# Performance work log

Measured on AMD Instinct MI355X. Metric: run time of the kernel, lower is better.

The kernel has to match this reference:

```python
import jax, jax.numpy as jnp
import numpy as np

N, E = 50000, 800000          # nodes, edges
D_IN, D_HID, D_OUT = 128, 128, 64


def setup_inputs() -> dict:
    key = jax.random.key(0)
    ks = jax.random.split(key, 8)
    init = lambda k, s: (jax.random.normal(k, s, jnp.float32) / np.sqrt(s[0]).astype(np.float32))
    return dict(
        x=jax.random.normal(ks[0], (N, D_IN), jnp.float32),
        edge_index=jax.random.randint(ks[1], (2, E), 0, N, dtype=jnp.int64),
        edge_attr=jax.random.uniform(ks[2], (E,), jnp.float32),
        W1=init(ks[3], (D_IN, D_HID)), b1=jnp.zeros((D_HID,), jnp.float32),
        W2=init(ks[4], (D_HID, D_HID)), b2=jnp.zeros((D_HID,), jnp.float32),
        Wmu=init(ks[5], (D_HID, D_OUT)), bmu=jnp.zeros((D_OUT,), jnp.float32),
        Wstd=init(ks[6], (D_HID, D_OUT)), bstd=jnp.zeros((D_OUT,), jnp.float32),
    )


def gcn_conv(x, src, dst, ew, W, b):
    """PyG GCNConv: symmetric-normalized aggregation with self-loops (weight 1).
    Self-loop contribution handled analytically (dinv[i]^2 * h[i]) to avoid
    concatenating N extra edges."""
    h = x @ W                                              # [N, Dout]
    deg = jax.ops.segment_sum(ew, dst, num_segments=N) + 1.0   # +1 for self-loop
    dinv = jnp.where(deg > 0, deg ** -0.5, 0.0)            # D^{-1/2}
    norm = dinv[src] * ew * dinv[dst]                      # [E]
    agg = jax.ops.segment_sum(h[src] * norm[:, None], dst, num_segments=N)
    agg = agg + h * (dinv * dinv)[:, None]                 # self-loop term
    return agg + b


def reference(x, edge_index, edge_attr, W1, b1, W2, b2, Wmu, bmu, Wstd, bstd):
    src, dst = edge_index[0], edge_index[1]
    h = jax.nn.relu(gcn_conv(x, src, dst, edge_attr, W1, b1))   # encoder layer 1
    h = gcn_conv(h, src, dst, edge_attr, W2, b2)                # encoder layer 2
    h = jax.nn.relu(h)                                          # .relu() in forward
    mu = gcn_conv(h, src, dst, edge_attr, Wmu, bmu)
    std = gcn_conv(h, src, dst, edge_attr, Wstd, bstd)
    return mu, std
```

## Files before the change

kernel.cpp:

```cpp
#include <hip/hip_runtime.h>
#include <math.h>

static constexpr int N = 50000;
static constexpr int E = 800000;
static constexpr int D = 128;
static constexpr int DO = 64;
static constexpr int CAP = 64;

__device__ __forceinline__ unsigned pack_bf16(float a, float b) {
  unsigned ua = __float_as_uint(a), ub = __float_as_uint(b);
  ua = (ua + 0x7FFFu + ((ua >> 16) & 1u)) >> 16;
  ub = (ub + 0x7FFFu + ((ub >> 16) & 1u)) >> 16;
  return ua | (ub << 16);
}
__device__ __forceinline__ float blo(unsigned u) { return __uint_as_float(u << 16); }
__device__ __forceinline__ float bhi(unsigned u) { return __uint_as_float(u & 0xFFFF0000u); }

typedef __attribute__((ext_vector_type(8))) short bf16x8;
typedef __attribute__((ext_vector_type(4))) float f32x4;

__global__ __launch_bounds__(256) void k_zero(int* __restrict__ cnt) {
  int i = blockIdx.x * 256 + threadIdx.x;
  if (i < N) cnt[i] = 0;
}

__global__ __launch_bounds__(256) void k_build_ell(const int* __restrict__ src,
                                                   const int* __restrict__ dst,
                                                   const float* __restrict__ ew,
                                                   int* __restrict__ cnt,
                                                   int2* __restrict__ ell) {
  int e = blockIdx.x * 256 + threadIdx.x;
  if (e >= E) return;
  int s = src[e], d = dst[e];
  int pos = __hip_atomic_fetch_add(&cnt[d], 1, __ATOMIC_RELAXED, __HIP_MEMORY_SCOPE_AGENT);
  if (pos < CAP)
    ell[(size_t)d * CAP + pos] = make_int2(s, __float_as_int(ew[e]));
}

__global__ __launch_bounds__(256) void k_degcast(const float* __restrict__ x,
                                                 const int* __restrict__ cnt,
                                                 const int2* __restrict__ ell,
                                                 float* __restrict__ dinv,
                                                 unsigned* __restrict__ bhs) {
  int node = blockIdx.x * 4 + (threadIdx.x >> 6);
  if (node >= N) return;
  int lane = threadIdx.x & 63;

  int len = cnt[node];
  float sum = (lane < len) ? __int_as_float(ell[(size_t)node * CAP + lane].y) : 0.f;
#pragma unroll
  for (int off = 1; off < 64; off <<= 1) sum += __shfl_xor(sum, off, 64);

  float dv = 1.0f / sqrtf(1.0f + sum);
  if (lane == 0) dinv[node] = dv;

  float2 v = ((const float2*)x)[(size_t)node * 64 + lane];
  bhs[(size_t)node * 64 + lane] = pack_bf16(v.x * dv, v.y * dv);
}

__device__ __forceinline__ float2 agg_core(const unsigned* __restrict__ bp,
                                           const int2* __restrict__ ell,
                                           int node, int len, float s) {
  unsigned hb = bp[(size_t)node * 64];
  float ax = blo(hb), ay = bhi(hb);

  const int2* row = ell + (size_t)node * CAP;
  int e = 0;
  for (; e + 8 <= len; e += 8) {
    int4 p0 = *(const int4*)(row + e + 0);
    int4 p1 = *(const int4*)(row + e + 2);
    int4 p2 = *(const int4*)(row + e + 4);
    int4 p3 = *(const int4*)(row + e + 6);
    unsigned b0 = bp[(size_t)p0.x * 64];
    unsigned b1 = bp[(size_t)p0.z * 64];
    unsigned b2 = bp[(size_t)p1.x * 64];
    unsigned b3 = bp[(size_t)p1.z * 64];
    unsigned b4 = bp[(size_t)p2.x * 64];
    unsigned b5 = bp[(size_t)p2.z * 64];
    unsigned b6 = bp[(size_t)p3.x * 64];
    unsigned b7 = bp[(size_t)p3.z * 64];
    float w0 = __int_as_float(p0.y), w1 = __int_as_float(p0.w);
    float w2 = __int_as_float(p1.y), w3 = __int_as_float(p1.w);
    float w4 = __int_as_float(p2.y), w5 = __int_as_float(p2.w);
    float w6 = __int_as_float(p3.y), w7 = __int_as_float(p3.w);
    ax = fmaf(blo(b0), w0, ax); ay = fmaf(bhi(b0), w0, ay);
    ax = fmaf(blo(b1), w1, ax); ay = fmaf(bhi(b1), w1, ay);
    ax = fmaf(blo(b2), w2, ax); ay = fmaf(bhi(b2), w2, ay);
    ax = fmaf(blo(b3), w3, ax); ay = fmaf(bhi(b3), w3, ay);
    ax = fmaf(blo(b4), w4, ax); ay = fmaf(bhi(b4), w4, ay);
    ax = fmaf(blo(b5), w5, ax); ay = fmaf(bhi(b5), w5, ay);
    ax = fmaf(blo(b6), w6, ax); ay = fmaf(bhi(b6), w6, ay);
    ax = fmaf(blo(b7), w7, ax); ay = fmaf(bhi(b7), w7, ay);
  }
  for (; e + 2 <= len; e += 2) {
    int4 p0 = *(const int4*)(row + e);
    unsigned b0 = bp[(size_t)p0.x * 64];
    unsigned b1 = bp[(size_t)p0.z * 64];
    float w0 = __int_as_float(p0.y), w1 = __int_as_float(p0.w);
    ax = fmaf(blo(b0), w0, ax); ay = fmaf(bhi(b0), w0, ay);
    ax = fmaf(blo(b1), w1, ax); ay = fmaf(bhi(b1), w1, ay);
  }
  if (e < len) {
    int2 pe = row[e];
    float w = __int_as_float(pe.y);
    unsigned b = bp[(size_t)pe.x * 64];
    ax = fmaf(blo(b), w, ax); ay = fmaf(bhi(b), w, ay);
  }
  float2 r; r.x = ax * s; r.y = ay * s;
  return r;
}

__global__ __launch_bounds__(1024) void k_layer_fused(const unsigned* __restrict__ bhs,
                                                      const int* __restrict__ cnt,
                                                      const int2* __restrict__ ell,
                                                      const float* __restrict__ dinv,
                                                      const float* __restrict__ W,
                                                      const float* __restrict__ bias,
                                                      unsigned* __restrict__ outb) {
  __shared__ __align__(16) unsigned Al[64][68];
  __shared__ __align__(16) unsigned Wt[128][72];
  const int tid = threadIdx.x;
  const int row0 = blockIdx.x * 64;

  {
    int col = tid & 127, seg = tid >> 7;
#pragma unroll
    for (int m = 0; m < 8; ++m) {
      int k2 = seg * 8 + m;
      float w0 = W[(size_t)(2 * k2) * 128 + col];
      float w1 = W[(size_t)(2 * k2 + 1) * 128 + col];
      Wt[col][k2] = pack_bf16(w0, w1);
    }
  }

  const int w = tid >> 6, l = tid & 63;
#pragma unroll 1
  for (int i = 0; i < 4; ++i) {
    int r = 4 * w + i;
    int node = row0 + r;
    unsigned val = 0u;
    if (node < N) {
      float2 rr = agg_core(bhs + l, ell, node, cnt[node], dinv[node]);
      val = pack_bf16(rr.x, rr.y);
    }
    Al[r][l] = val;
  }
  __syncthreads();

  const int c = l & 15, q = l >> 4;
#pragma unroll
  for (int t2 = 0; t2 < 2; ++t2) {
    int t = 2 * w + t2;
    int rt = t >> 3, ct = t & 7;
    f32x4 acc = {};
#pragma unroll
    for (int ks = 0; ks < 4; ++ks) {
      bf16x8 af = *(const bf16x8*)&Al[rt * 16 + c][ks * 16 + 4 * q];
      bf16x8 bf = *(const bf16x8*)&Wt[ct * 16 + c][ks * 16 + 4 * q];
      acc = __builtin_amdgcn_mfma_f32_16x16x32_bf16(af, bf, acc, 0, 0, 0);
    }
    int col = ct * 16 + c;
    float bb = bias[col];
#pragma unroll
    for (int j = 0; j < 4; ++j) {
      int row = row0 + rt * 16 + 4 * q + j;
      float v = 0.f;
      if (row < N) v = fmaxf(acc[j] + bb, 0.f) * dinv[row];
      float o = __shfl_xor(v, 1);
      if (((c & 1) == 0) && row < N)
        outb[(size_t)row * 64 + (col >> 1)] = pack_bf16(v, o);
    }
  }
}

__global__ __launch_bounds__(1024) void k_head_fused(const unsigned* __restrict__ bhs,
                                                     const int* __restrict__ cnt,
                                                     const int2* __restrict__ ell,
                                                     const float* __restrict__ dinv,
                                                     const float* __restrict__ Wmu,
                                                     const float* __restrict__ Wstd,
                                                     const float* __restrict__ bmu,
                                                     const float* __restrict__ bstd,
                                                     float* __restrict__ out) {
  __shared__ __align__(16) unsigned Al[64][68];
  __shared__ __align__(16) unsigned Wt[128][72];
  const int tid = threadIdx.x;
  const int row0 = blockIdx.x * 64;

  {
    int col = tid & 127, seg = tid >> 7;
    const float* base = (col < DO) ? Wmu : Wstd;
    int cc = (col < DO) ? col : (col - DO);
#pragma unroll
    for (int m = 0; m < 8; ++m) {
      int k2 = seg * 8 + m;
      float w0 = base[(size_t)(2 * k2) * DO + cc];
      float w1 = base[(size_t)(2 * k2 + 1) * DO + cc];
      Wt[col][k2] = pack_bf16(w0, w1);
    }
  }

  const int w = tid >> 6, l = tid & 63;
#pragma unroll 1
  for (int i = 0; i < 4; ++i) {
    int r = 4 * w + i;
    int node = row0 + r;
    unsigned val = 0u;
    if (node < N) {
      float2 rr = agg_core(bhs + l, ell, node, cnt[node], dinv[node]);
      val = pack_bf16(rr.x, rr.y);
    }
    Al[r][l] = val;
  }
  __syncthreads();

  const int c = l & 15, q = l >> 4;
#pragma unroll
  for (int t2 = 0; t2 < 2; ++t2) {
    int t = 2 * w + t2;
    int rt = t >> 3, ct = t & 7;
    f32x4 acc = {};
#pragma unroll
    for (int ks = 0; ks < 4; ++ks) {
      bf16x8 af = *(const bf16x8*)&Al[rt * 16 + c][ks * 16 + 4 * q];
      bf16x8 bf = *(const bf16x8*)&Wt[ct * 16 + c][ks * 16 + 4 * q];
      acc = __builtin_amdgcn_mfma_f32_16x16x32_bf16(af, bf, acc, 0, 0, 0);
    }
    int col = ct * 16 + c;
    const bool is_mu = (col < DO);
    float bb = is_mu ? bmu[col] : bstd[col - DO];
    float* base = is_mu ? out : (out + (size_t)N * DO);
    int cc = is_mu ? col : (col - DO);
#pragma unroll
    for (int j = 0; j < 4; ++j) {
      int row = row0 + rt * 16 + 4 * q + j;
      if (row < N) base[(size_t)row * DO + cc] = acc[j] + bb;
    }
  }
}


static inline char* align256(char* p) {
  return (char*)(((uintptr_t)p + 255) & ~(uintptr_t)255);
}

extern "C" void kernel_launch(void* const* d_in, const int* in_sizes, int n_in,
                              void* d_out, int out_size, void* d_ws, size_t ws_size,
                              hipStream_t stream) {
  const float* x    = (const float*)d_in[0];
  const int*   ei   = (const int*)d_in[1];
  const float* ew   = (const float*)d_in[2];
  const float* W1   = (const float*)d_in[3];
  const float* b1   = (const float*)d_in[4];
  const float* W2   = (const float*)d_in[5];
  const float* b2   = (const float*)d_in[6];
  const float* Wmu  = (const float*)d_in[7];
  const float* bmu  = (const float*)d_in[8];
  const float* Wstd = (const float*)d_in[9];
  const float* bstd = (const float*)d_in[10];
  float* out = (float*)d_out;

  const int* srcI = ei;
  const int* dstI = ei + E;

  char* p = (char*)d_ws;
  float*    dinv = (float*)p;     p = align256(p + (size_t)N * 4);
  int*      cnt  = (int*)p;       p = align256(p + (size_t)N * 4);
  int2*     ell  = (int2*)p;      p = align256(p + (size_t)N * CAP * 8);
  unsigned* bhs  = (unsigned*)p;  p = align256(p + (size_t)N * 64 * 4);
  unsigned* bh2  = (unsigned*)p;  p = align256(p + (size_t)N * 64 * 4);

  dim3 blk(256);
  const int gN    = (N + 255) / 256;
  const int gE    = (E + 255) / 256;
  const int gAgg  = (N + 3) / 4;
  const int gFuse = (N + 63) / 64;

  k_zero<<<gN, blk, 0, stream>>>(cnt);
  k_build_ell<<<gE, blk, 0, stream>>>(srcI, dstI, ew, cnt, ell);
  k_degcast<<<gAgg, blk, 0, stream>>>(x, cnt, ell, dinv, bhs);

  k_layer_fused<<<gFuse, dim3(1024), 0, stream>>>(bhs, cnt, ell, dinv, W1, b1, bh2);
  k_layer_fused<<<gFuse, dim3(1024), 0, stream>>>(bh2, cnt, ell, dinv, W2, b2, bhs);
  k_head_fused<<<gFuse, dim3(1024), 0, stream>>>(bhs, cnt, ell, dinv, Wmu, Wstd, bmu, bstd, out);
}
```

Before: 200.8 us.

## Pack ELL entries into 32 bits with 16-bit index and fp16 weight

Each ELL entry shrinks from 8 bytes (int src plus float weight) to a single 32-bit word holding the low 16 bits of the source index and an fp16 edge weight. This halves the adjacency traffic in the degree and aggregation kernels and lets each uint4 load cover four neighbours. The ELL build kernel also handles four edges per thread to batch its atomics. Since N is 50000, node indices above 65535 would be truncated; they fit for this size, but the format is fixed to N below 65536, and storing weights in fp16 loses some precision.

```diff
diff --git a/kernel.cpp b/kernel.cpp
--- a/kernel.cpp
+++ b/kernel.cpp
@@ -1,4 +1,5 @@
 #include <hip/hip_runtime.h>
+#include <hip/hip_fp16.h>
 #include <math.h>
 
 static constexpr int N = 50000;
@@ -16,6 +17,13 @@
 __device__ __forceinline__ float blo(unsigned u) { return __uint_as_float(u << 16); }
 __device__ __forceinline__ float bhi(unsigned u) { return __uint_as_float(u & 0xFFFF0000u); }
 
+__device__ __forceinline__ unsigned ell_pack(int s, float w) {
+  return (unsigned)s | ((unsigned)__half_as_ushort(__float2half(w)) << 16);
+}
+__device__ __forceinline__ float ell_w(unsigned p) {
+  return __half2float(__ushort_as_half((unsigned short)(p >> 16)));
+}
+
 typedef __attribute__((ext_vector_type(8))) short bf16x8;
 typedef __attribute__((ext_vector_type(4))) float f32x4;
 
@@ -28,18 +36,31 @@
                                                    const int* __restrict__ dst,
                                                    const float* __restrict__ ew,
                                                    int* __restrict__ cnt,
-                                                   int2* __restrict__ ell) {
-  int e = blockIdx.x * 256 + threadIdx.x;
-  if (e >= E) return;
-  int s = src[e], d = dst[e];
-  int pos = __hip_atomic_fetch_add(&cnt[d], 1, __ATOMIC_RELAXED, __HIP_MEMORY_SCOPE_AGENT);
-  if (pos < CAP)
-    ell[(size_t)d * CAP + pos] = make_int2(s, __float_as_int(ew[e]));
+                                                   unsigned* __restrict__ ell) {
+  int e0 = blockIdx.x * 1024 + threadIdx.x;
+  int d[4], s[4];
+  float w[4];
+  bool ok[4];
+#pragma unroll
+  for (int i = 0; i < 4; ++i) {
+    int e = e0 + i * 256;
+    ok[i] = (e < E);
+    if (ok[i]) { d[i] = dst[e]; s[i] = src[e]; w[i] = ew[e]; }
+  }
+  int pos[4];
+#pragma unroll
+  for (int i = 0; i < 4; ++i)
+    if (ok[i])
+      pos[i] = __hip_atomic_fetch_add(&cnt[d[i]], 1, __ATOMIC_RELAXED, __HIP_MEMORY_SCOPE_AGENT);
+#pragma unroll
+  for (int i = 0; i < 4; ++i)
+    if (ok[i] && pos[i] < CAP)
+      ell[(size_t)d[i] * CAP + pos[i]] = ell_pack(s[i], w[i]);
 }
 
 __global__ __launch_bounds__(256) void k_degcast(const float* __restrict__ x,
                                                  const int* __restrict__ cnt,
-                                                 const int2* __restrict__ ell,
+                                                 const unsigned* __restrict__ ell,
                                                  float* __restrict__ dinv,
                                                  unsigned* __restrict__ bhs) {
   int node = blockIdx.x * 4 + (threadIdx.x >> 6);
@@ -47,7 +68,7 @@
   int lane = threadIdx.x & 63;
 
   int len = cnt[node];
-  float sum = (lane < len) ? __int_as_float(ell[(size_t)node * CAP + lane].y) : 0.f;
+  float sum = (lane < len) ? ell_w(ell[(size_t)node * CAP + lane]) : 0.f;
 #pragma unroll
   for (int off = 1; off < 64; off <<= 1) sum += __shfl_xor(sum, off, 64);
 
@@ -59,30 +80,26 @@
 }
 
 __device__ __forceinline__ float2 agg_core(const unsigned* __restrict__ bp,
-                                           const int2* __restrict__ ell,
+                                           const unsigned* __restrict__ ell,
                                            int node, int len, float s) {
   unsigned hb = bp[(size_t)node * 64];
   float ax = blo(hb), ay = bhi(hb);
 
-  const int2* row = ell + (size_t)node * CAP;
+  const unsigned* row = ell + (size_t)node * CAP;
   int e = 0;
   for (; e + 8 <= len; e += 8) {
-    int4 p0 = *(const int4*)(row + e + 0);
-    int4 p1 = *(const int4*)(row + e + 2);
-    int4 p2 = *(const int4*)(row + e + 4);
-    int4 p3 = *(const int4*)(row + e + 6);
-    unsigned b0 = bp[(size_t)p0.x * 64];
-    unsigned b1 = bp[(size_t)p0.z * 64];
-    unsigned b2 = bp[(size_t)p1.x * 64];
-    unsigned b3 = bp[(size_t)p1.z * 64];
-    unsigned b4 = bp[(size_t)p2.x * 64];
-    unsigned b5 = bp[(size_t)p2.z * 64];
-    unsigned b6 = bp[(size_t)p3.x * 64];
-    unsigned b7 = bp[(size_t)p3.z * 64];
-    float w0 = __int_as_float(p0.y), w1 = __int_as_float(p0.w);
-    float w2 = __int_as_float(p1.y), w3 = __int_as_float(p1.w);
-    float w4 = __int_as_float(p2.y), w5 = __int_as_float(p2.w);
-    float w6 = __int_as_float(p3.y), w7 = __int_as_float(p3.w);
+    uint4 p0 = *(const uint4*)(row + e);
+    uint4 p1 = *(const uint4*)(row + e + 4);
+    unsigned b0 = bp[(size_t)(p0.x & 0xFFFFu) * 64];
+    unsigned b1 = bp[(size_t)(p0.y & 0xFFFFu) * 64];
+    unsigned b2 = bp[(size_t)(p0.z & 0xFFFFu) * 64];
+    unsigned b3 = bp[(size_t)(p0.w & 0xFFFFu) * 64];
+    unsigned b4 = bp[(size_t)(p1.x & 0xFFFFu) * 64];
+    unsigned b5 = bp[(size_t)(p1.y & 0xFFFFu) * 64];
+    unsigned b6 = bp[(size_t)(p1.z & 0xFFFFu) * 64];
+    unsigned b7 = bp[(size_t)(p1.w & 0xFFFFu) * 64];
+    float w0 = ell_w(p0.x), w1 = ell_w(p0.y), w2 = ell_w(p0.z), w3 = ell_w(p0.w);
+    float w4 = ell_w(p1.x), w5 = ell_w(p1.y), w6 = ell_w(p1.z), w7 = ell_w(p1.w);
     ax = fmaf(blo(b0), w0, ax); ay = fmaf(bhi(b0), w0, ay);
     ax = fmaf(blo(b1), w1, ax); ay = fmaf(bhi(b1), w1, ay);
     ax = fmaf(blo(b2), w2, ax); ay = fmaf(bhi(b2), w2, ay);
@@ -92,18 +109,23 @@
     ax = fmaf(blo(b6), w6, ax); ay = fmaf(bhi(b6), w6, ay);
     ax = fmaf(blo(b7), w7, ax); ay = fmaf(bhi(b7), w7, ay);
   }
-  for (; e + 2 <= len; e += 2) {
-    int4 p0 = *(const int4*)(row + e);
-    unsigned b0 = bp[(size_t)p0.x * 64];
-    unsigned b1 = bp[(size_t)p0.z * 64];
-    float w0 = __int_as_float(p0.y), w1 = __int_as_float(p0.w);
+  if (e + 4 <= len) {
+    uint4 p0 = *(const uint4*)(row + e);
+    unsigned b0 = bp[(size_t)(p0.x & 0xFFFFu) * 64];
+    unsigned b1 = bp[(size_t)(p0.y & 0xFFFFu) * 64];
+    unsigned b2 = bp[(size_t)(p0.z & 0xFFFFu) * 64];
+    unsigned b3 = bp[(size_t)(p0.w & 0xFFFFu) * 64];
+    float w0 = ell_w(p0.x), w1 = ell_w(p0.y), w2 = ell_w(p0.z), w3 = ell_w(p0.w);
     ax = fmaf(blo(b0), w0, ax); ay = fmaf(bhi(b0), w0, ay);
     ax = fmaf(blo(b1), w1, ax); ay = fmaf(bhi(b1), w1, ay);
-  }
-  if (e < len) {
-    int2 pe = row[e];
-    float w = __int_as_float(pe.y);
-    unsigned b = bp[(size_t)pe.x * 64];
+    ax = fmaf(blo(b2), w2, ax); ay = fmaf(bhi(b2), w2, ay);
+    ax = fmaf(blo(b3), w3, ax); ay = fmaf(bhi(b3), w3, ay);
+    e += 4;
+  }
+  for (; e < len; ++e) {
+    unsigned pe = row[e];
+    float w = ell_w(pe);
+    unsigned b = bp[(size_t)(pe & 0xFFFFu) * 64];
     ax = fmaf(blo(b), w, ax); ay = fmaf(bhi(b), w, ay);
   }
   float2 r; r.x = ax * s; r.y = ay * s;
@@ -112,7 +134,7 @@
 
 __global__ __launch_bounds__(1024) void k_layer_fused(const unsigned* __restrict__ bhs,
                                                       const int* __restrict__ cnt,
-                                                      const int2* __restrict__ ell,
+                                                      const unsigned* __restrict__ ell,
                                                       const float* __restrict__ dinv,
                                                       const float* __restrict__ W,
                                                       const float* __restrict__ bias,
@@ -175,7 +197,7 @@
 
 __global__ __launch_bounds__(1024) void k_head_fused(const unsigned* __restrict__ bhs,
                                                      const int* __restrict__ cnt,
-                                                     const int2* __restrict__ ell,
+                                                     const unsigned* __restrict__ ell,
                                                      const float* __restrict__ dinv,
                                                      const float* __restrict__ Wmu,
                                                      const float* __restrict__ Wstd,
@@ -266,18 +288,18 @@
   char* p = (char*)d_ws;
   float*    dinv = (float*)p;     p = align256(p + (size_t)N * 4);
   int*      cnt  = (int*)p;       p = align256(p + (size_t)N * 4);
-  int2*     ell  = (int2*)p;      p = align256(p + (size_t)N * CAP * 8);
+  unsigned* ell  = (unsigned*)p;  p = align256(p + (size_t)N * CAP * 4);
   unsigned* bhs  = (unsigned*)p;  p = align256(p + (size_t)N * 64 * 4);
   unsigned* bh2  = (unsigned*)p;  p = align256(p + (size_t)N * 64 * 4);
 
   dim3 blk(256);
-  const int gN    = (N + 255) / 256;
-  const int gE    = (E + 255) / 256;
-  const int gAgg  = (N + 3) / 4;
-  const int gFuse = (N + 63) / 64;
+  const int gN     = (N + 255) / 256;
+  const int gBuild = (E + 1023) / 1024;
+  const int gAgg   = (N + 3) / 4;
+  const int gFuse  = (N + 63) / 64;
 
   k_zero<<<gN, blk, 0, stream>>>(cnt);
-  k_build_ell<<<gE, blk, 0, stream>>>(srcI, dstI, ew, cnt, ell);
+  k_build_ell<<<gBuild, blk, 0, stream>>>(srcI, dstI, ew, cnt, ell);
   k_degcast<<<gAgg, blk, 0, stream>>>(x, cnt, ell, dinv, bhs);
 
   k_layer_fused<<<gFuse, dim3(1024), 0, stream>>>(bhs, cnt, ell, dinv, W1, b1, bh2);
```

Result: faster. 193.1 us (-3.8%).
